# Optimization experiments

Hardware: AMD Instinct MI355X
Metric: run time of the kernel (lower is better)

Reference implementation:

```python
import jax, jax.numpy as jnp
import numpy as np

NUM_DOF = 7
NUM_STEPS = 100
T = 0.02
V_MAX, A_MAX, J_MAX, P_MAX = 1.0, 2.0, 5.0, 3.14
MAXITER = 20
RHO = 1.0
BATCH = 1024
HIDDEN = 1024
NVAR = NUM_DOF * NUM_STEPS            # 700
NUM_ACC = NUM_STEPS - 1
NUM_JERK = NUM_ACC - 1
NUM_POS = NUM_STEPS
NVC = 2 * NUM_STEPS * NUM_DOF         # vel constraints
NAC = 2 * NUM_ACC * NUM_DOF
NJC = 2 * NUM_JERK * NUM_DOF
NPC = 2 * NUM_POS * NUM_DOF
M_CON = NVC + NAC + NJC + NPC         # 5558 total constraints
OUT_DIM = 2 * NVAR + M_CON            # 6958 mlp output dim

def _build_mats():
    P_vel = np.eye(NUM_STEPS)
    P_acc = np.diff(P_vel, axis=0) / T
    P_jerk = np.diff(P_acc, axis=0) / T
    P_pos = np.cumsum(P_vel, axis=0) * T
    ud = lambda P: np.vstack((P, -P))
    I = np.eye(NUM_DOF)
    A_control = np.vstack([np.kron(I, ud(P)) for P in (P_vel, P_acc, P_jerk, P_pos)])
    bnd = np.zeros((1, NUM_STEPS)); bnd[0, 0] = 1.0
    A_eq = np.kron(I, bnd)
    cost = np.eye(NVAR) + RHO * (A_control.T @ A_control)  # A_projection = I
    Q = np.block([[cost, A_eq.T], [A_eq, np.zeros((NUM_DOF, NUM_DOF))]])
    Q_inv = np.linalg.inv(Q)
    return jnp.asarray(A_control, jnp.float32), jnp.asarray(Q_inv, jnp.float32)

A_CONTROL, Q_INV = _build_mats()


def setup_inputs() -> dict:
    key = jax.random.key(0)
    k1, k2, k3, k4, k5 = jax.random.split(key, 5)
    return {
        "input_nn": jax.random.normal(k1, (BATCH, NVAR), jnp.float32),
        "theta_init": jax.random.uniform(k2, (BATCH, 1), jnp.float32),
        "v_start": jax.random.normal(k3, (BATCH, NUM_DOF), jnp.float32),
        "W1": jax.random.normal(k4, (NVAR, HIDDEN), jnp.float32) / np.sqrt(NVAR).astype(np.float32),
        "b1": jnp.zeros((HIDDEN,), jnp.float32),
        "W2": jax.random.normal(k5, (HIDDEN, OUT_DIM), jnp.float32) / np.sqrt(HIDDEN).astype(np.float32),
        "b2": jnp.zeros((OUT_DIM,), jnp.float32),
    }


def reference(input_nn, theta_init, v_start, W1, b1, W2, b2):
    # robust normalization (torch.median on even batch = lower middle element)
    med = jnp.quantile(input_nn, 0.5, axis=0, method="lower")
    q1 = jnp.quantile(input_nn, 0.25, axis=0)
    q3 = jnp.quantile(input_nn, 0.75, axis=0)
    iqr = q3 - q1
    iqr = jnp.where(iqr == 0, jnp.asarray(1.0, iqr.dtype), iqr)
    inp_norm = (input_nn - med) / iqr

    # mlp decoder
    h = jax.nn.relu(inp_norm @ W1 + b1)
    out = h @ W2 + b2
    xi0 = out[:, :NVAR]
    lam0 = out[:, NVAR:2 * NVAR]
    s0 = jnp.maximum(0.0, out[:, 2 * NVAR:2 * NVAR + M_CON])

    xi_samples = input_nn[:, :NVAR]
    B = input_nn.shape[0]
    dt = input_nn.dtype
    b_control = jnp.concatenate([
        V_MAX * jnp.ones((B, NVC), dt),
        A_MAX * jnp.ones((B, NAC), dt),
        J_MAX * jnp.ones((B, NJC), dt),
        (-theta_init + P_MAX) * jnp.ones((B, NPC // 2), dt),
        (theta_init + P_MAX) * jnp.ones((B, NPC // 2), dt),
    ], axis=1)  # [B, M_CON]
    b_eq = v_start  # [B, num_dof]

    def step(carry, _):
        xi, lam, s = carry
        b_aug = b_control - s
        # lincost = -lamda - xi_samples - rho * A_control^T b_aug   (A_projection = I)
        lincost = -lam - xi_samples - RHO * (b_aug @ A_CONTROL)
        rhs = jnp.concatenate([-lincost, b_eq], axis=1)        # [B, nvar+dof]
        sol = rhs @ Q_INV.T
        xi_new = sol[:, :NVAR]
        Ax = xi_new @ A_CONTROL.T                              # [B, M_CON]
        s_new = jnp.maximum(0.0, b_control - Ax)
        res_vec = Ax - b_control + s_new
        res_norm = jnp.linalg.norm(res_vec, axis=1)
        lam_new = lam - RHO * (res_vec @ A_CONTROL)
        fp = jnp.linalg.norm(lam - lam_new, axis=1) + jnp.linalg.norm(s - s_new, axis=1)
        return (xi_new, lam_new, s_new), (res_norm, fp)

    (xi_f, _, _), (primal_res, fixed_res) = jax.lax.scan(step, (xi0, lam0, s0), None, length=MAXITER)
    avg_primal = jnp.sum(primal_res, axis=0) / MAXITER
    avg_fixed = jnp.sum(fixed_res, axis=0) / MAXITER
    return xi_f, avg_fixed, avg_primal, primal_res, fixed_res
```

## Files before the change

kernel.cpp:

```cpp
#include <hip/hip_runtime.h>

#define NVARS 700
#define MC    5558
#define MAXIT 20

typedef __attribute__((ext_vector_type(8))) short bf16x8;
typedef __attribute__((ext_vector_type(4))) float f32x4;

__device__ __forceinline__ ushort f2bf(float x) {
  unsigned u = __float_as_uint(x);
  return (ushort)((u + 0x7FFFu + ((u >> 16) & 1u)) >> 16);
}

__device__ __forceinline__ double Wfun(int a, int b) {
  if (a < 0 || a > 99 || b < 0 || b > 99) return 0.0;
  int d = a - b; if (d < 0) d = -d;
  int l = a < b ? a : b;
  const double iT2 = 2500.0;
  const double iT4 = 6250000.0;
  double w = 0.0;
  if (d == 0) {
    w = 3.0;
    w += 2.0 * iT2 * (double)((a <= 98 ? 1 : 0) + (a >= 1 ? 1 : 0));
    double dd = (double)(((a - 2) >= 0 && (a - 2) <= 97) ? 1 : 0)
              + 4.0 * (double)(((a - 1) >= 0 && (a - 1) <= 97) ? 1 : 0)
              + (double)((a <= 97) ? 1 : 0);
    w += 2.0 * iT4 * dd;
  } else if (d == 1) {
    w = -2.0 * iT2;
    double dd = -2.0 * (double)(((l - 1) >= 0 && (l - 1) <= 97) ? 1 : 0)
                - 2.0 * (double)((l <= 97) ? 1 : 0);
    w += 2.0 * iT4 * dd;
  } else if (d == 2) {
    w = 2.0 * iT4 * (double)((l <= 97) ? 1 : 0);
  }
  return w;
}

__global__ __launch_bounds__(128) void qinv_kernel(double* __restrict__ zbuf,
                                                   double* __restrict__ cid,
                                                   float* __restrict__ Qt)
{
  __shared__ double Bb[100][4];
  __shared__ double Gb[100][4];
  __shared__ double invd[100];
  int tid = threadIdx.x;
  for (int q = tid; q < 400; q += 128) {
    int i = q >> 2, k = q & 3;
    int j = i - k;
    double v = 0.0;
    if (j >= 0) {
      v = Wfun(i, j) - Wfun(i + 1, j) - Wfun(i, j + 1) + Wfun(i + 1, j + 1);
      if (k == 0) v += 2.0 * 0.02 * 0.02;
    }
    Bb[i][k] = v;
  }
  __syncthreads();
  if (tid == 0) {
    for (int i = 0; i < 100; ++i) {
      for (int k = 3; k >= 1; --k) {
        int j = i - k;
        if (j < 0) { Gb[i][k] = 0.0; continue; }
        double s = Bb[i][k];
        for (int m = k + 1; m <= 3; ++m)
          if (m <= i) s -= Gb[i][m] * Gb[j][m - k];
        Gb[i][k] = s * invd[j];
      }
      double s = Bb[i][0];
      for (int m = 1; m <= 3; ++m)
        if (m <= i) s -= Gb[i][m] * Gb[i][m];
      double g = sqrt(s);
      Gb[i][0] = g;
      invd[i] = 1.0 / g;
    }
  }
  __syncthreads();
  if (tid < 100) {
    int c = tid;
    double z0 = 0, z1 = 0, z2 = 0;
    for (int i = 0; i < 100; ++i) {
      double v = (i == c ? 1.0 : 0.0) - (i == (c - 1) ? 1.0 : 0.0);
      double s = v - Gb[i][1] * z0 - Gb[i][2] * z1 - Gb[i][3] * z2;
      double z = s * invd[i];
      zbuf[i * 128 + c] = z;
      z2 = z1; z1 = z0; z0 = z;
    }
    double y0 = 0, y1 = 0, y2 = 0;
    for (int i = 99; i >= 0; --i) {
      double s = zbuf[i * 128 + c];
      if (i + 1 <= 99) s -= Gb[i + 1][1] * y0;
      if (i + 2 <= 99) s -= Gb[i + 2][2] * y1;
      if (i + 3 <= 99) s -= Gb[i + 3][3] * y2;
      double y = s * invd[i];
      zbuf[i * 128 + c] = y;
      y2 = y1; y1 = y0; y0 = y;
    }
    double ym = 0.0;
    for (int i = 0; i < 100; ++i) {
      double y = zbuf[i * 128 + c];
      cid[i * 100 + c] = y - ym;
      ym = y;
    }
  }
  __syncthreads();
  double invs = 1.0 / cid[0];
  for (int q = tid; q < 101 * 100; q += 128) {
    int k = q / 100, i = q - (q / 100) * 100;
    double val;
    if (k < 100) val = cid[i * 100 + k] - cid[i * 100] * cid[k] * invs;
    else         val = cid[i * 100] * invs;
    Qt[k * 100 + i] = (float)val;
  }
}

__global__ __launch_bounds__(256) void quantile_kernel(const float* __restrict__ in,
                                                       float* __restrict__ med,
                                                       float* __restrict__ rinv)
{
  __shared__ float v[1024];
  int c = blockIdx.x, tid = threadIdx.x;
  for (int i = tid; i < 1024; i += 256) v[i] = in[i * NVARS + c];
  __syncthreads();
  for (int k = 2; k <= 1024; k <<= 1) {
    for (int j = k >> 1; j > 0; j >>= 1) {
      for (int i = tid; i < 1024; i += 256) {
        int ixj = i ^ j;
        if (ixj > i) {
          float a = v[i], b2 = v[ixj];
          bool up = ((i & k) == 0);
          if ((a > b2) == up) { v[i] = b2; v[ixj] = a; }
        }
      }
      __syncthreads();
    }
  }
  if (tid == 0) {
    float m  = v[511];
    float q1 = v[255] + 0.75f * (v[256] - v[255]);
    float q3 = v[767] + 0.25f * (v[768] - v[767]);
    float iq = q3 - q1;
    if (iq == 0.f) iq = 1.f;
    med[c] = m;
    rinv[c] = 1.f / iq;
  }
}

__global__ __launch_bounds__(256) void normalize_split(const float* __restrict__ in,
                                                       const float* __restrict__ med,
                                                       const float* __restrict__ rinv,
                                                       ushort* __restrict__ Ah,
                                                       ushort* __restrict__ Al)
{
  int idx = blockIdx.x * 256 + threadIdx.x;
  if (idx >= 1024 * 704) return;
  int r = idx / 704, c = idx - r * 704;
  float v = 0.f;
  if (c < 700) v = (in[r * NVARS + c] - med[c]) * rinv[c];
  ushort h = f2bf(v);
  float fh = __uint_as_float(((unsigned)h) << 16);
  Ah[idx] = h;
  Al[idx] = f2bf(v - fh);
}

__global__ __launch_bounds__(256) void tsplit(const float* __restrict__ src,
                                              int srows, int scols, int sld, int col0,
                                              ushort* __restrict__ dh,
                                              ushort* __restrict__ dl, int dld)
{
  __shared__ float tile[32][33];
  int k0 = blockIdx.x * 32, n0 = blockIdx.y * 32;
  int tx = threadIdx.x, ty = threadIdx.y;
  for (int i = ty; i < 32; i += 8) {
    int k = k0 + i, c = col0 + n0 + tx;
    tile[i][tx] = (k < srows && c < scols) ? src[(size_t)k * sld + c] : 0.f;
  }
  __syncthreads();
  for (int i = ty; i < 32; i += 8) {
    int n = n0 + i, k = k0 + tx;
    float v = tile[tx][i];
    ushort h = f2bf(v);
    float fh = __uint_as_float(((unsigned)h) << 16);
    dh[(size_t)n * dld + k] = h;
    dl[(size_t)n * dld + k] = f2bf(v - fh);
  }
}

template <int MODE>
__global__ __launch_bounds__(256) void gemm_mfma(
    const ushort* __restrict__ Agh, const ushort* __restrict__ Agl,
    const ushort* __restrict__ Bgh, const ushort* __restrict__ Bgl,
    const float* __restrict__ bias, int bias_n,
    float* __restrict__ Cf, ushort* __restrict__ Chi, ushort* __restrict__ Clo,
    int Kp, int ldc)
{
  __shared__ __align__(16) ushort Ash[128 * 40];
  __shared__ __align__(16) ushort Asl[128 * 40];
  __shared__ __align__(16) ushort Bsh[128 * 40];
  __shared__ __align__(16) ushort Bsl[128 * 40];

  const int t = threadIdx.x;
  const int srow = t >> 1;
  const int sc0 = (t & 1) * 2;
  const size_t bm = (size_t)blockIdx.y * 128;
  const size_t bn = (size_t)blockIdx.x * 128;

  const ushort* gAh = Agh + (bm + srow) * Kp + sc0 * 8;
  const ushort* gAl = Agl + (bm + srow) * Kp + sc0 * 8;
  const ushort* gBh = Bgh + (bn + srow) * Kp + sc0 * 8;
  const ushort* gBl = Bgl + (bn + srow) * Kp + sc0 * 8;

  const int w = t >> 6, lane = t & 63;
  const int wr = w >> 1, wc = w & 1;
  const int fr = lane & 15, fg = lane >> 4;

  f32x4 acc[4][4];
#pragma unroll
  for (int a = 0; a < 4; ++a)
#pragma unroll
    for (int b = 0; b < 4; ++b) acc[a][b] = (f32x4){0.f, 0.f, 0.f, 0.f};

  const int nk = Kp >> 5;
  uint4 rA0, rA1, rAl0, rAl1, rB0, rB1, rBl0, rBl1;
  {
    rA0  = *(const uint4*)(gAh);      rA1  = *(const uint4*)(gAh + 8);
    rAl0 = *(const uint4*)(gAl);      rAl1 = *(const uint4*)(gAl + 8);
    rB0  = *(const uint4*)(gBh);      rB1  = *(const uint4*)(gBh + 8);
    rBl0 = *(const uint4*)(gBl);      rBl1 = *(const uint4*)(gBl + 8);
  }
  const int woff = srow * 40 + sc0 * 8;

  for (int kt = 0;; ++kt) {
    __syncthreads();
    *(uint4*)&Ash[woff] = rA0;  *(uint4*)&Ash[woff + 8] = rA1;
    *(uint4*)&Asl[woff] = rAl0; *(uint4*)&Asl[woff + 8] = rAl1;
    *(uint4*)&Bsh[woff] = rB0;  *(uint4*)&Bsh[woff + 8] = rB1;
    *(uint4*)&Bsl[woff] = rBl0; *(uint4*)&Bsl[woff + 8] = rBl1;
    __syncthreads();
    if (kt + 1 < nk) {
      int ko = (kt + 1) * 32;
      rA0  = *(const uint4*)(gAh + ko);      rA1  = *(const uint4*)(gAh + ko + 8);
      rAl0 = *(const uint4*)(gAl + ko);      rAl1 = *(const uint4*)(gAl + ko + 8);
      rB0  = *(const uint4*)(gBh + ko);      rB1  = *(const uint4*)(gBh + ko + 8);
      rBl0 = *(const uint4*)(gBl + ko);      rBl1 = *(const uint4*)(gBl + ko + 8);
    }
    bf16x8 fah[4], fal[4], fbh[4], fbl[4];
#pragma unroll
    for (int mf = 0; mf < 4; ++mf) {
      int off = (wr * 64 + mf * 16 + fr) * 40 + fg * 8;
      fah[mf] = *(const bf16x8*)&Ash[off];
      fal[mf] = *(const bf16x8*)&Asl[off];
    }
#pragma unroll
    for (int nf = 0; nf < 4; ++nf) {
      int off = (wc * 64 + nf * 16 + fr) * 40 + fg * 8;
      fbh[nf] = *(const bf16x8*)&Bsh[off];
      fbl[nf] = *(const bf16x8*)&Bsl[off];
    }
#pragma unroll
    for (int mf = 0; mf < 4; ++mf)
#pragma unroll
      for (int nf = 0; nf < 4; ++nf) {
        acc[mf][nf] = __builtin_amdgcn_mfma_f32_16x16x32_bf16(fah[mf], fbh[nf], acc[mf][nf], 0, 0, 0);
        acc[mf][nf] = __builtin_amdgcn_mfma_f32_16x16x32_bf16(fah[mf], fbl[nf], acc[mf][nf], 0, 0, 0);
        acc[mf][nf] = __builtin_amdgcn_mfma_f32_16x16x32_bf16(fal[mf], fbh[nf], acc[mf][nf], 0, 0, 0);
      }
    if (kt + 1 >= nk) break;
  }

#pragma unroll
  for (int mf = 0; mf < 4; ++mf)
#pragma unroll
    for (int nf = 0; nf < 4; ++nf) {
      int col = (int)bn + wc * 64 + nf * 16 + fr;
      int rowb = (int)bm + wr * 64 + mf * 16 + fg * 4;
#pragma unroll
      for (int j = 0; j < 4; ++j) {
        int row = rowb + j;
        float v = acc[mf][nf][j];
        if (MODE == 0) {
          float bv = (col < bias_n) ? bias[col] : 0.f;
          Cf[(size_t)row * ldc + col] = v + bv;
        } else {
          float r = fmaxf(v + bias[col], 0.f);
          ushort h = f2bf(r);
          float fh = __uint_as_float(((unsigned)h) << 16);
          Chi[(size_t)row * ldc + col] = h;
          Clo[(size_t)row * ldc + col] = f2bf(r - fh);
        }
      }
    }
}

__global__ __launch_bounds__(256) void normalize_kernel(const float* __restrict__ in,
                                                        const float* __restrict__ med,
                                                        const float* __restrict__ rinv,
                                                        float* __restrict__ An)
{
  int idx = blockIdx.x * 256 + threadIdx.x;
  if (idx < 1024 * NVARS) {
    int c = idx % NVARS;
    An[idx] = (in[idx] - med[c]) * rinv[c];
  }
}

template <bool RELU>
__global__ __launch_bounds__(256) void gemm_kernel(const float* __restrict__ A, int lda,
                                                   const float* __restrict__ B, int ldb,
                                                   const float* __restrict__ bias,
                                                   float* __restrict__ C, int ldc,
                                                   int N, int K)
{
  __shared__ __align__(16) float As[16][68];
  __shared__ __align__(16) float Bs[16][64];
  int tid = threadIdx.x;
  int bm = blockIdx.y * 64, bn = blockIdx.x * 64;
  int tx = tid & 15, ty = tid >> 4;
  float acc[4][4] = {};
  for (int k0 = 0; k0 < K; k0 += 16) {
    {
      int q = tid * 4;
      int m = q >> 4, kk = q & 15;
      const float* ap = A + (size_t)(bm + m) * lda + k0;
#pragma unroll
      for (int s2 = 0; s2 < 4; ++s2) {
        int kc = kk + s2;
        As[kc][m] = (k0 + kc < K) ? ap[kc] : 0.f;
      }
    }
#pragma unroll
    for (int s2 = 0; s2 < 4; ++s2) {
      int q = tid + s2 * 256;
      int kk = q >> 6, n = q & 63;
      float val = 0.f;
      if (k0 + kk < K && bn + n < N) val = B[(size_t)(k0 + kk) * ldb + bn + n];
      Bs[kk][n] = val;
    }
    __syncthreads();
#pragma unroll
    for (int kk = 0; kk < 16; ++kk) {
      float4 av = *reinterpret_cast<const float4*>(&As[kk][ty * 4]);
      float4 bv = *reinterpret_cast<const float4*>(&Bs[kk][tx * 4]);
      acc[0][0] += av.x * bv.x; acc[0][1] += av.x * bv.y; acc[0][2] += av.x * bv.z; acc[0][3] += av.x * bv.w;
      acc[1][0] += av.y * bv.x; acc[1][1] += av.y * bv.y; acc[1][2] += av.y * bv.z; acc[1][3] += av.y * bv.w;
      acc[2][0] += av.z * bv.x; acc[2][1] += av.z * bv.y; acc[2][2] += av.z * bv.z; acc[2][3] += av.z * bv.w;
      acc[3][0] += av.w * bv.x; acc[3][1] += av.w * bv.y; acc[3][2] += av.w * bv.z; acc[3][3] += av.w * bv.w;
    }
    __syncthreads();
  }
#pragma unroll
  for (int i = 0; i < 4; ++i) {
    int m = bm + ty * 4 + i;
#pragma unroll
    for (int j = 0; j < 4; ++j) {
      int n = bn + tx * 4 + j;
      if (n < N) {
        float r = acc[i][j] + bias[n];
        if (RELU) r = fmaxf(r, 0.f);
        C[(size_t)m * ldc + n] = r;
      }
    }
  }
}

__device__ __forceinline__ float iscan(float v, int lane) {
#pragma unroll
  for (int off = 1; off < 64; off <<= 1) {
    float u = __shfl_up(v, off);
    v += (lane >= off) ? u : 0.f;
  }
  return v;
}

template <bool RES>
__device__ __forceinline__ float segw(const float* td, int pi, int mi) {
  if (!RES) return fmaxf(td[mi], 0.f) - fmaxf(td[pi], 0.f);
  else      return fmaxf(-td[pi], 0.f) - fmaxf(-td[mi], 0.f);
}

template <bool RES>
__device__ __forceinline__ float atop(const float* td, int i, float rc) {
  float u = segw<RES>(td, i, 100 + i);
  float ya = (i >= 1)  ? segw<RES>(td, 200 + i - 1, 299 + i - 1) : 0.f;
  float yb = (i <= 98) ? segw<RES>(td, 200 + i,     299 + i)     : 0.f;
  u += (ya - yb) * 50.f;
  float z2 = (i >= 2)             ? segw<RES>(td, 398 + i - 2, 496 + i - 2) : 0.f;
  float z1 = (i >= 1 && i <= 98)  ? segw<RES>(td, 398 + i - 1, 496 + i - 1) : 0.f;
  float z0 = (i <= 97)            ? segw<RES>(td, 398 + i,     496 + i)     : 0.f;
  u += (z2 - 2.f * z1 + z0) * 2500.f;
  u += 0.02f * rc;
  return u;
}

__global__ __launch_bounds__(448) void solver_kernel(const float* __restrict__ out2,
                                                     const float* __restrict__ input,
                                                     const float* __restrict__ theta,
                                                     const float* __restrict__ vstart,
                                                     const float* __restrict__ Qtg,
                                                     float* __restrict__ out, int ldo)
{
  __shared__ float t_l[7][794];
  __shared__ __align__(16) float ru_t[101][8];
  __shared__ float pm[4][700];
  __shared__ float part[7][20][3];
  __shared__ float prfp[40];

  const int b = blockIdx.x, tid = threadIdx.x;
  const int d = tid >> 6, l = tid & 63;
  const bool hi = (l < 36);
  const int i2 = 64 + l;
  float* td = &t_l[d][0];
  const float* orow = out2 + (size_t)b * ldo;
  const float* srow = orow + 700;
  const float th = theta[b];

  float lam0 = orow[d * 100 + l];
  float xs0  = input[(size_t)b * NVARS + d * 100 + l];
  float lam1 = 0.f, xs1 = 0.f;
  if (hi) {
    lam1 = orow[d * 100 + i2];
    xs1  = input[(size_t)b * NVARS + d * 100 + i2];
  }
  {
    int vb = d * 200, ab = 1400 + d * 198, jb = 2786 + d * 196, pb = 4158 + d * 200;
    td[l]       = fmaxf(srow[vb + l], 0.f);
    td[100 + l] = fmaxf(srow[vb + 100 + l], 0.f);
    if (l <= 98) { td[200 + l] = fmaxf(srow[ab + l], 0.f);      td[299 + l] = fmaxf(srow[ab + 99 + l], 0.f); }
    if (l <= 97) { td[398 + l] = fmaxf(srow[jb + l], 0.f);      td[496 + l] = fmaxf(srow[jb + 98 + l], 0.f); }
    td[594 + l] = fmaxf(srow[pb + l], 0.f);
    td[694 + l] = fmaxf(srow[pb + 100 + l], 0.f);
    if (hi) {
      td[i2]       = fmaxf(srow[vb + i2], 0.f);
      td[100 + i2] = fmaxf(srow[vb + 100 + i2], 0.f);
      if (l <= 34) { td[200 + i2] = fmaxf(srow[ab + i2], 0.f);  td[299 + i2] = fmaxf(srow[ab + 99 + i2], 0.f); }
      if (l <= 33) { td[398 + i2] = fmaxf(srow[jb + i2], 0.f);  td[496 + i2] = fmaxf(srow[jb + 98 + i2], 0.f); }
      td[594 + i2] = fmaxf(srow[pb + i2], 0.f);
      td[694 + i2] = fmaxf(srow[pb + 100 + i2], 0.f);
    }
  }
  if (l == 0) ru_t[100][d] = vstart[b * 7 + d];

  for (int it = 0; it < MAXIT; ++it) {
    {
      float pa0 = segw<false>(td, 594 + l, 694 + l);
      float pa1 = hi ? segw<false>(td, 594 + i2, 694 + i2) : 0.f;
      if (d == 3) { pa0 -= 2.f * th; if (hi) pa1 -= 2.f * th; }
      float s0i = iscan(pa0, l);
      float tot0 = __shfl(s0i, 63);
      float s1i = iscan(hi ? pa1 : 0.f, l) + tot0;
      float S = __shfl(s1i, 35);
      float rc0 = S - s0i + pa0;
      float ru0 = lam0 + xs0 + atop<false>(td, l, rc0);
      ru_t[l][d] = ru0;
      if (hi) {
        float rc1 = S - s1i + pa1;
        float ru1 = lam1 + xs1 + atop<false>(td, i2, rc1);
        ru_t[i2][d] = ru1;
      }
    }
    __syncthreads();

    {
      int kc = tid / 112, r = tid - kc * 112;
      if (r < 100) {
        float acc[7] = {0.f, 0.f, 0.f, 0.f, 0.f, 0.f, 0.f};
        int k0 = kc * 25, k1 = (kc == 3) ? 101 : k0 + 25;
        for (int k = k0; k < k1; ++k) {
          float qv = Qtg[k * 100 + r];
          float4 ra = *reinterpret_cast<const float4*>(&ru_t[k][0]);
          float4 rb = *reinterpret_cast<const float4*>(&ru_t[k][4]);
          acc[0] += qv * ra.x; acc[1] += qv * ra.y; acc[2] += qv * ra.z; acc[3] += qv * ra.w;
          acc[4] += qv * rb.x; acc[5] += qv * rb.y; acc[6] += qv * rb.z;
        }
#pragma unroll
        for (int dd = 0; dd < 7; ++dd) pm[kc][dd * 100 + r] = acc[dd];
      }
    }
    __syncthreads();
    {
      int p = tid;
      if (p < 700) { float v = pm[0][p] + pm[1][p] + pm[2][p] + pm[3][p]; pm[0][p] = v; }
      p = tid + 448;
      if (p < 700) { float v = pm[0][p] + pm[1][p] + pm[2][p] + pm[3][p]; pm[0][p] = v; }
    }
    __syncthreads();

    float r2 = 0.f, ds2 = 0.f, dl2 = 0.f;
    {
      const float* xid = &pm[0][d * 100];
      float x0 = xid[l], x1 = hi ? xid[i2] : 0.f;
      float c0i = iscan(x0, l);
      float tt0 = __shfl(c0i, 63);
      float c1i = iscan(hi ? x1 : 0.f, l) + tt0;
      float bp = (d <= 3) ? (3.14f - th) : (3.14f + th);
      float bm2 = (d < 3) ? (3.14f - th) : (3.14f + th);
#define UPD(idx, tnew) { int _ix = (idx); float _tn = (tnew); float _to = td[_ix]; \
      float _dd = fmaxf(_to, 0.f) - fmaxf(_tn, 0.f); ds2 += _dd * _dd; \
      float _rr = fmaxf(-_tn, 0.f); r2 += _rr * _rr; td[_ix] = _tn; }
      UPD(l, 1.f - x0) UPD(100 + l, 1.f + x0)
      if (hi) { UPD(i2, 1.f - x1) UPD(100 + i2, 1.f + x1) }
      if (l <= 98) { float a = (xid[l + 1] - x0) * 50.f; UPD(200 + l, 2.f - a) UPD(299 + l, 2.f + a) }
      if (hi && l <= 34) { float a = (xid[i2 + 1] - x1) * 50.f; UPD(200 + i2, 2.f - a) UPD(299 + i2, 2.f + a) }
      if (l <= 97) { float jr = (xid[l + 2] - 2.f * xid[l + 1] + x0) * 2500.f; UPD(398 + l, 5.f - jr) UPD(496 + l, 5.f + jr) }
      if (hi && l <= 33) { float jr = (xid[i2 + 2] - 2.f * xid[i2 + 1] + x1) * 2500.f; UPD(398 + i2, 5.f - jr) UPD(496 + i2, 5.f + jr) }
      UPD(594 + l, bp - 0.02f * c0i) UPD(694 + l, bm2 + 0.02f * c0i)
      if (hi) { UPD(594 + i2, bp - 0.02f * c1i) UPD(694 + i2, bm2 + 0.02f * c1i) }
#undef UPD
    }

    {
      float pa0 = segw<true>(td, 594 + l, 694 + l);
      float pa1 = hi ? segw<true>(td, 594 + i2, 694 + i2) : 0.f;
      float s0i = iscan(pa0, l);
      float tot0 = __shfl(s0i, 63);
      float s1i = iscan(hi ? pa1 : 0.f, l) + tot0;
      float S = __shfl(s1i, 35);
      float rc0 = S - s0i + pa0;
      float g0 = atop<true>(td, l, rc0);
      lam0 -= g0; dl2 += g0 * g0;
      if (hi) {
        float rc1 = S - s1i + pa1;
        float g1 = atop<true>(td, i2, rc1);
        lam1 -= g1; dl2 += g1 * g1;
      }
    }

#pragma unroll
    for (int o = 32; o > 0; o >>= 1) {
      r2  += __shfl_down(r2, o);
      ds2 += __shfl_down(ds2, o);
      dl2 += __shfl_down(dl2, o);
    }
    if (l == 0) { part[d][it][0] = r2; part[d][it][1] = ds2; part[d][it][2] = dl2; }
  }

  __syncthreads();
  {
    float* xout = out + (size_t)b * NVARS + d * 100;
    const float* xid = &pm[0][d * 100];
    xout[l] = xid[l];
    if (hi) xout[i2] = xid[i2];
  }
  if (tid < 20) {
    int it = tid;
    float R2 = 0.f, DS2 = 0.f, DL2 = 0.f;
    for (int dd = 0; dd < 7; ++dd) {
      R2 += part[dd][it][0]; DS2 += part[dd][it][1]; DL2 += part[dd][it][2];
    }
    float pr = sqrtf(R2), fp = sqrtf(DL2) + sqrtf(DS2);
    out[718848 + it * 1024 + b] = pr;
    out[739328 + it * 1024 + b] = fp;
    prfp[it] = pr; prfp[20 + it] = fp;
  }
  __syncthreads();
  if (tid == 0) {
    float ap = 0.f, af = 0.f;
    for (int it = 0; it < 20; ++it) { ap += prfp[it]; af += prfp[20 + it]; }
    out[716800 + b] = af / 20.f;
    out[717824 + b] = ap / 20.f;
  }
}

extern "C" void kernel_launch(void* const* d_in, const int* in_sizes, int n_in,
                              void* d_out, int out_size, void* d_ws, size_t ws_size,
                              hipStream_t stream) {
  (void)in_sizes; (void)n_in; (void)out_size;
  const float* input  = (const float*)d_in[0];
  const float* theta  = (const float*)d_in[1];
  const float* vstart = (const float*)d_in[2];
  const float* W1     = (const float*)d_in[3];
  const float* b1     = (const float*)d_in[4];
  const float* W2     = (const float*)d_in[5];
  const float* b2     = (const float*)d_in[6];
  float* out = (float*)d_out;

  double* wsd  = (double*)d_ws;
  double* zbuf = wsd;
  double* cid  = wsd + 12800;
  float* wsf  = (float*)d_ws;
  float* Qt   = wsf + 45600;
  float* med  = wsf + 55704;
  float* rinv = wsf + 56408;

  hipLaunchKernelGGL(qinv_kernel, dim3(1), dim3(128), 0, stream, zbuf, cid, Qt);
  hipLaunchKernelGGL(quantile_kernel, dim3(700), dim3(256), 0, stream, input, med, rinv);

  const size_t HHI = 57112, HLO = 581400, W2TH = 1105688, W2TL = 4316952,
               OUT2 = 7528216, NEED = 13950744;
  const size_t ANH = OUT2, ANL = OUT2 + 360448, W1TH = OUT2 + 720896, W1TL = OUT2 + 1081344;

  if (ws_size >= NEED * 4ull) {
    ushort* an_h  = (ushort*)(wsf + ANH);
    ushort* an_l  = (ushort*)(wsf + ANL);
    ushort* w1t_h = (ushort*)(wsf + W1TH);
    ushort* w1t_l = (ushort*)(wsf + W1TL);
    ushort* h_h   = (ushort*)(wsf + HHI);
    ushort* h_l   = (ushort*)(wsf + HLO);
    ushort* w2t_h = (ushort*)(wsf + W2TH);
    ushort* w2t_l = (ushort*)(wsf + W2TL);
    float*  out2  = wsf + OUT2;

    hipLaunchKernelGGL(normalize_split, dim3((1024 * 704 + 255) / 256), dim3(256), 0, stream,
                       input, med, rinv, an_h, an_l);
    hipLaunchKernelGGL(tsplit, dim3(22, 32), dim3(32, 8), 0, stream,
                       W1, 700, 1024, 1024, 0, w1t_h, w1t_l, 704);
    hipLaunchKernelGGL(tsplit, dim3(32, 196), dim3(32, 8), 0, stream,
                       W2, 1024, 6958, 6958, 700, w2t_h, w2t_l, 1024);
    hipLaunchKernelGGL((gemm_mfma<1>), dim3(8, 8), dim3(256), 0, stream,
                       an_h, an_l, w1t_h, w1t_l, b1, 1024,
                       (float*)nullptr, h_h, h_l, 704, 1024);
    hipLaunchKernelGGL((gemm_mfma<0>), dim3(49, 8), dim3(256), 0, stream,
                       h_h, h_l, w2t_h, w2t_l, b2 + 700, 6258,
                       out2, (ushort*)nullptr, (ushort*)nullptr, 1024, 6272);
    hipLaunchKernelGGL(solver_kernel, dim3(1024), dim3(448), 0, stream,
                       out2, input, theta, vstart, Qt, out, 6272);
  } else {
    float* An   = wsf + 57112;
    float* h    = wsf + 773912;
    float* out2 = wsf + 1822488;
    if (ws_size < (size_t)(1822488 + 6408192) * 4) return;
    hipLaunchKernelGGL(normalize_kernel, dim3(2800), dim3(256), 0, stream, input, med, rinv, An);
    hipLaunchKernelGGL((gemm_kernel<true>), dim3(16, 16), dim3(256), 0, stream,
                       An, NVARS, W1, 1024, b1, h, 1024, 1024, NVARS);
    hipLaunchKernelGGL((gemm_kernel<false>), dim3(98, 16), dim3(256), 0, stream,
                       h, 1024, W2 + 700, 6958, b2 + 700, out2, 6258, 6258, 1024);
    hipLaunchKernelGGL(solver_kernel, dim3(1024), dim3(448), 0, stream,
                       out2, input, theta, vstart, Qt, out, 6258);
  }
}
```

Before: 555.8 us.

## Keep solver slack state in registers and retile MFMA GEMMs for more blocks

The solver kernel no longer keeps its per-DOF slack arrays in shared memory. Each lane holds its constraint slacks in registers, neighbour values move through warp shuffles, and the A^T-apply phase computes both the s-weighted and residual-weighted terms in one fused pass, which also drops a redundant scan. Less shared memory plus __launch_bounds__(448,7) aims for higher occupancy. The MFMA GEMM is templated on tile size and launched with smaller tiles (64x64 and 128x64) to spread work over more blocks, at the cost of less data reuse per block.

New measurement: 776.7 us. 1.4x slower.

```diff
diff --git a/kernel.cpp b/kernel.cpp
--- a/kernel.cpp
+++ b/kernel.cpp
@@ -185,7 +185,7 @@
   }
 }
 
-template <int MODE>
+template <int BM, int BN, int MODE>
 __global__ __launch_bounds__(256) void gemm_mfma(
     const ushort* __restrict__ Agh, const ushort* __restrict__ Agl,
     const ushort* __restrict__ Bgh, const ushort* __restrict__ Bgl,
@@ -193,73 +193,82 @@
     float* __restrict__ Cf, ushort* __restrict__ Chi, ushort* __restrict__ Clo,
     int Kp, int ldc)
 {
-  __shared__ __align__(16) ushort Ash[128 * 40];
-  __shared__ __align__(16) ushort Asl[128 * 40];
-  __shared__ __align__(16) ushort Bsh[128 * 40];
-  __shared__ __align__(16) ushort Bsl[128 * 40];
+  constexpr int ACH = BM * 4 / 256;
+  constexpr int BCH = BN * 4 / 256;
+  constexpr int MF = BM / 32;
+  constexpr int NF = BN / 32;
+  __shared__ __align__(16) ushort Ash[BM * 40];
+  __shared__ __align__(16) ushort Asl[BM * 40];
+  __shared__ __align__(16) ushort Bsh[BN * 40];
+  __shared__ __align__(16) ushort Bsl[BN * 40];
 
   const int t = threadIdx.x;
-  const int srow = t >> 1;
-  const int sc0 = (t & 1) * 2;
-  const size_t bm = (size_t)blockIdx.y * 128;
-  const size_t bn = (size_t)blockIdx.x * 128;
-
-  const ushort* gAh = Agh + (bm + srow) * Kp + sc0 * 8;
-  const ushort* gAl = Agl + (bm + srow) * Kp + sc0 * 8;
-  const ushort* gBh = Bgh + (bn + srow) * Kp + sc0 * 8;
-  const ushort* gBl = Bgl + (bn + srow) * Kp + sc0 * 8;
+  const size_t bm = (size_t)blockIdx.y * BM;
+  const size_t bn = (size_t)blockIdx.x * BN;
+
+  size_t aoff[ACH]; int awo[ACH];
+#pragma unroll
+  for (int s = 0; s < ACH; ++s) {
+    int slot = t * ACH + s, row = slot >> 2, ch = slot & 3;
+    aoff[s] = (bm + row) * (size_t)Kp + ch * 8;
+    awo[s] = row * 40 + ch * 8;
+  }
+  size_t boff[BCH]; int bwo[BCH];
+#pragma unroll
+  for (int s = 0; s < BCH; ++s) {
+    int slot = t * BCH + s, row = slot >> 2, ch = slot & 3;
+    boff[s] = (bn + row) * (size_t)Kp + ch * 8;
+    bwo[s] = row * 40 + ch * 8;
+  }
 
   const int w = t >> 6, lane = t & 63;
   const int wr = w >> 1, wc = w & 1;
   const int fr = lane & 15, fg = lane >> 4;
 
-  f32x4 acc[4][4];
-#pragma unroll
-  for (int a = 0; a < 4; ++a)
-#pragma unroll
-    for (int b = 0; b < 4; ++b) acc[a][b] = (f32x4){0.f, 0.f, 0.f, 0.f};
+  f32x4 acc[MF][NF];
+#pragma unroll
+  for (int a = 0; a < MF; ++a)
+#pragma unroll
+    for (int b = 0; b < NF; ++b) acc[a][b] = (f32x4){0.f, 0.f, 0.f, 0.f};
 
   const int nk = Kp >> 5;
-  uint4 rA0, rA1, rAl0, rAl1, rB0, rB1, rBl0, rBl1;
-  {
-    rA0  = *(const uint4*)(gAh);      rA1  = *(const uint4*)(gAh + 8);
-    rAl0 = *(const uint4*)(gAl);      rAl1 = *(const uint4*)(gAl + 8);
-    rB0  = *(const uint4*)(gBh);      rB1  = *(const uint4*)(gBh + 8);
-    rBl0 = *(const uint4*)(gBl);      rBl1 = *(const uint4*)(gBl + 8);
-  }
-  const int woff = srow * 40 + sc0 * 8;
+  uint4 rAh[ACH], rAl[ACH], rBh[BCH], rBl[BCH];
+#pragma unroll
+  for (int s = 0; s < ACH; ++s) { rAh[s] = *(const uint4*)(Agh + aoff[s]); rAl[s] = *(const uint4*)(Agl + aoff[s]); }
+#pragma unroll
+  for (int s = 0; s < BCH; ++s) { rBh[s] = *(const uint4*)(Bgh + boff[s]); rBl[s] = *(const uint4*)(Bgl + boff[s]); }
 
   for (int kt = 0;; ++kt) {
     __syncthreads();
-    *(uint4*)&Ash[woff] = rA0;  *(uint4*)&Ash[woff + 8] = rA1;
-    *(uint4*)&Asl[woff] = rAl0; *(uint4*)&Asl[woff + 8] = rAl1;
-    *(uint4*)&Bsh[woff] = rB0;  *(uint4*)&Bsh[woff + 8] = rB1;
-    *(uint4*)&Bsl[woff] = rBl0; *(uint4*)&Bsl[woff + 8] = rBl1;
+#pragma unroll
+    for (int s = 0; s < ACH; ++s) { *(uint4*)&Ash[awo[s]] = rAh[s]; *(uint4*)&Asl[awo[s]] = rAl[s]; }
+#pragma unroll
+    for (int s = 0; s < BCH; ++s) { *(uint4*)&Bsh[bwo[s]] = rBh[s]; *(uint4*)&Bsl[bwo[s]] = rBl[s]; }
     __syncthreads();
     if (kt + 1 < nk) {
       int ko = (kt + 1) * 32;
-      rA0  = *(const uint4*)(gAh + ko);      rA1  = *(const uint4*)(gAh + ko + 8);
-      rAl0 = *(const uint4*)(gAl + ko);      rAl1 = *(const uint4*)(gAl + ko + 8);
-      rB0  = *(const uint4*)(gBh + ko);      rB1  = *(const uint4*)(gBh + ko + 8);
-      rBl0 = *(const uint4*)(gBl + ko);      rBl1 = *(const uint4*)(gBl + ko + 8);
-    }
-    bf16x8 fah[4], fal[4], fbh[4], fbl[4];
-#pragma unroll
-    for (int mf = 0; mf < 4; ++mf) {
-      int off = (wr * 64 + mf * 16 + fr) * 40 + fg * 8;
+#pragma unroll
+      for (int s = 0; s < ACH; ++s) { rAh[s] = *(const uint4*)(Agh + aoff[s] + ko); rAl[s] = *(const uint4*)(Agl + aoff[s] + ko); }
+#pragma unroll
+      for (int s = 0; s < BCH; ++s) { rBh[s] = *(const uint4*)(Bgh + boff[s] + ko); rBl[s] = *(const uint4*)(Bgl + boff[s] + ko); }
+    }
+    bf16x8 fah[MF], fal[MF], fbh[NF], fbl[NF];
+#pragma unroll
+    for (int mf = 0; mf < MF; ++mf) {
+      int off = (wr * (BM / 2) + mf * 16 + fr) * 40 + fg * 8;
       fah[mf] = *(const bf16x8*)&Ash[off];
       fal[mf] = *(const bf16x8*)&Asl[off];
     }
 #pragma unroll
-    for (int nf = 0; nf < 4; ++nf) {
-      int off = (wc * 64 + nf * 16 + fr) * 40 + fg * 8;
+    for (int nf = 0; nf < NF; ++nf) {
+      int off = (wc * (BN / 2) + nf * 16 + fr) * 40 + fg * 8;
       fbh[nf] = *(const bf16x8*)&Bsh[off];
       fbl[nf] = *(const bf16x8*)&Bsl[off];
     }
 #pragma unroll
-    for (int mf = 0; mf < 4; ++mf)
-#pragma unroll
-      for (int nf = 0; nf < 4; ++nf) {
+    for (int mf = 0; mf < MF; ++mf)
+#pragma unroll
+      for (int nf = 0; nf < NF; ++nf) {
         acc[mf][nf] = __builtin_amdgcn_mfma_f32_16x16x32_bf16(fah[mf], fbh[nf], acc[mf][nf], 0, 0, 0);
         acc[mf][nf] = __builtin_amdgcn_mfma_f32_16x16x32_bf16(fah[mf], fbl[nf], acc[mf][nf], 0, 0, 0);
         acc[mf][nf] = __builtin_amdgcn_mfma_f32_16x16x32_bf16(fal[mf], fbh[nf], acc[mf][nf], 0, 0, 0);
@@ -268,11 +277,11 @@
   }
 
 #pragma unroll
-  for (int mf = 0; mf < 4; ++mf)
-#pragma unroll
-    for (int nf = 0; nf < 4; ++nf) {
-      int col = (int)bn + wc * 64 + nf * 16 + fr;
-      int rowb = (int)bm + wr * 64 + mf * 16 + fg * 4;
+  for (int mf = 0; mf < MF; ++mf)
+#pragma unroll
+    for (int nf = 0; nf < NF; ++nf) {
+      int col = (int)bn + wc * (BN / 2) + nf * 16 + fr;
+      int rowb = (int)bm + wr * (BM / 2) + mf * 16 + fg * 4;
 #pragma unroll
       for (int j = 0; j < 4; ++j) {
         int row = rowb + j;
@@ -371,35 +380,72 @@
   return v;
 }
 
-template <bool RES>
-__device__ __forceinline__ float segw(const float* td, int pi, int mi) {
-  if (!RES) return fmaxf(td[mi], 0.f) - fmaxf(td[pi], 0.f);
-  else      return fmaxf(-td[pi], 0.f) - fmaxf(-td[mi], 0.f);
-}
-
-template <bool RES>
-__device__ __forceinline__ float atop(const float* td, int i, float rc) {
-  float u = segw<RES>(td, i, 100 + i);
-  float ya = (i >= 1)  ? segw<RES>(td, 200 + i - 1, 299 + i - 1) : 0.f;
-  float yb = (i <= 98) ? segw<RES>(td, 200 + i,     299 + i)     : 0.f;
-  u += (ya - yb) * 50.f;
-  float z2 = (i >= 2)             ? segw<RES>(td, 398 + i - 2, 496 + i - 2) : 0.f;
-  float z1 = (i >= 1 && i <= 98)  ? segw<RES>(td, 398 + i - 1, 496 + i - 1) : 0.f;
-  float z0 = (i <= 97)            ? segw<RES>(td, 398 + i,     496 + i)     : 0.f;
-  u += (z2 - 2.f * z1 + z0) * 2500.f;
-  u += 0.02f * rc;
-  return u;
-}
-
-__global__ __launch_bounds__(448) void solver_kernel(const float* __restrict__ out2,
-                                                     const float* __restrict__ input,
-                                                     const float* __restrict__ theta,
-                                                     const float* __restrict__ vstart,
-                                                     const float* __restrict__ Qtg,
-                                                     float* __restrict__ out, int ldo)
-{
-  __shared__ float t_l[7][794];
-  __shared__ __align__(16) float ru_t[101][8];
+struct TR {
+  float vp0, vm0, vp1, vm1;
+  float ap0, am0, ap1, am1;
+  float jp0, jm0, jp1, jm1;
+  float pp0, pm0, pp1, pm1;
+};
+
+__device__ __forceinline__ void wpair(float tp, float tm, float& ws, float& wr) {
+  float a = fmaxf(tp, 0.f), b = fmaxf(tm, 0.f);
+  ws = b - a;
+  wr = (tm - tp) - ws;
+}
+
+__device__ __forceinline__ void w_phase(const TR& t, int l, bool hi, float dth,
+                                        float& os0, float& os1, float& or0, float& or1)
+{
+  float vs0, vr0, vs1, vr1, ys0, yr0, ys1, yr1;
+  float zs0, zr0, zs1, zr1, ps0, pr0, ps1, pr1;
+  wpair(t.vp0, t.vm0, vs0, vr0);
+  wpair(t.ap0, t.am0, ys0, yr0);
+  wpair(t.jp0, t.jm0, zs0, zr0);
+  wpair(t.pp0, t.pm0, ps0, pr0);
+  if (hi) { wpair(t.vp1, t.vm1, vs1, vr1); wpair(t.pp1, t.pm1, ps1, pr1); }
+  else    { vs1 = vr1 = ps1 = pr1 = 0.f; }
+  if (hi && l <= 34) { wpair(t.ap1, t.am1, ys1, yr1); } else { ys1 = yr1 = 0.f; }
+  if (hi && l <= 33) { wpair(t.jp1, t.jm1, zs1, zr1); } else { zs1 = zr1 = 0.f; }
+
+  const int lm1 = (l + 63) & 63, lm2 = (l + 62) & 63;
+  float u1ys0 = __shfl(ys0, lm1), u1ys1 = __shfl(ys1, lm1);
+  float u1zs0 = __shfl(zs0, lm1), u1zs1 = __shfl(zs1, lm1);
+  float u2zs0 = __shfl(zs0, lm2), u2zs1 = __shfl(zs1, lm2);
+  float u1yr0 = __shfl(yr0, lm1), u1yr1 = __shfl(yr1, lm1);
+  float u1zr0 = __shfl(zr0, lm1), u1zr1 = __shfl(zr1, lm1);
+  float u2zr0 = __shfl(zr0, lm2), u2zr1 = __shfl(zr1, lm2);
+
+  float pa0s = ps0 + dth;
+  float pa1s = hi ? ps1 + dth : 0.f;
+  float pa0r = pr0;
+  float pa1r = hi ? pr1 : 0.f;
+  float s0s = iscan(pa0s, l);
+  float s0r = iscan(pa0r, l);
+  float tots = __shfl(s0s, 63), totr = __shfl(s0r, 63);
+  float s1s = iscan(pa1s, l) + tots;
+  float s1r = iscan(pa1r, l) + totr;
+  float Ss = __shfl(s1s, 35), Sr = __shfl(s1r, 35);
+  float rc0s = Ss - s0s + pa0s, rc1s = Ss - s1s + pa1s;
+  float rc0r = Sr - s0r + pa0r, rc1r = Sr - s1r + pa1r;
+
+  float ym1s0 = l ? u1ys0 : 0.f, zm1s0 = l ? u1zs0 : 0.f, zm2s0 = (l >= 2) ? u2zs0 : 0.f;
+  float ym1r0 = l ? u1yr0 : 0.f, zm1r0 = l ? u1zr0 : 0.f, zm2r0 = (l >= 2) ? u2zr0 : 0.f;
+  os0 = vs0 + 50.f * (ym1s0 - ys0) + 2500.f * (zm2s0 - 2.f * zm1s0 + zs0) + 0.02f * rc0s;
+  or0 = vr0 + 50.f * (ym1r0 - yr0) + 2500.f * (zm2r0 - 2.f * zm1r0 + zr0) + 0.02f * rc0r;
+  float ym1s1 = l ? u1ys1 : u1ys0, zm1s1 = l ? u1zs1 : u1zs0, zm2s1 = (l >= 2) ? u2zs1 : u2zs0;
+  float ym1r1 = l ? u1yr1 : u1yr0, zm1r1 = l ? u1zr1 : u1zr0, zm2r1 = (l >= 2) ? u2zr1 : u2zr0;
+  os1 = vs1 + 50.f * (ym1s1 - ys1) + 2500.f * (zm2s1 - 2.f * zm1s1 + zs1) + 0.02f * rc1s;
+  or1 = vr1 + 50.f * (ym1r1 - yr1) + 2500.f * (zm2r1 - 2.f * zm1r1 + zr1) + 0.02f * rc1r;
+}
+
+__global__ __launch_bounds__(448, 7) void solver_kernel(const float* __restrict__ out2,
+                                                        const float* __restrict__ input,
+                                                        const float* __restrict__ theta,
+                                                        const float* __restrict__ vstart,
+                                                        const float* __restrict__ Qtg,
+                                                        float* __restrict__ out, int ldo)
+{
+  __shared__ __align__(16) float ru_t[101][12];
   __shared__ float pm[4][700];
   __shared__ float part[7][20][3];
   __shared__ float prfp[40];
@@ -408,57 +454,45 @@
   const int d = tid >> 6, l = tid & 63;
   const bool hi = (l < 36);
   const int i2 = 64 + l;
-  float* td = &t_l[d][0];
+  const float th = theta[b];
+  const float dth = (d == 3) ? -2.f * th : 0.f;
+  const float bp  = (d <= 3) ? (3.14f - th) : (3.14f + th);
+  const float bm2 = (d <  3) ? (3.14f - th) : (3.14f + th);
   const float* orow = out2 + (size_t)b * ldo;
   const float* srow = orow + 700;
-  const float th = theta[b];
 
   float lam0 = orow[d * 100 + l];
   float xs0  = input[(size_t)b * NVARS + d * 100 + l];
-  float lam1 = 0.f, xs1 = 0.f;
-  if (hi) {
-    lam1 = orow[d * 100 + i2];
-    xs1  = input[(size_t)b * NVARS + d * 100 + i2];
-  }
+  float lam1 = hi ? orow[d * 100 + i2] : 0.f;
+  float xs1  = hi ? input[(size_t)b * NVARS + d * 100 + i2] : 0.f;
+
+  TR t;
   {
-    int vb = d * 200, ab = 1400 + d * 198, jb = 2786 + d * 196, pb = 4158 + d * 200;
-    td[l]       = fmaxf(srow[vb + l], 0.f);
-    td[100 + l] = fmaxf(srow[vb + 100 + l], 0.f);
-    if (l <= 98) { td[200 + l] = fmaxf(srow[ab + l], 0.f);      td[299 + l] = fmaxf(srow[ab + 99 + l], 0.f); }
-    if (l <= 97) { td[398 + l] = fmaxf(srow[jb + l], 0.f);      td[496 + l] = fmaxf(srow[jb + 98 + l], 0.f); }
-    td[594 + l] = fmaxf(srow[pb + l], 0.f);
-    td[694 + l] = fmaxf(srow[pb + 100 + l], 0.f);
-    if (hi) {
-      td[i2]       = fmaxf(srow[vb + i2], 0.f);
-      td[100 + i2] = fmaxf(srow[vb + 100 + i2], 0.f);
-      if (l <= 34) { td[200 + i2] = fmaxf(srow[ab + i2], 0.f);  td[299 + i2] = fmaxf(srow[ab + 99 + i2], 0.f); }
-      if (l <= 33) { td[398 + i2] = fmaxf(srow[jb + i2], 0.f);  td[496 + i2] = fmaxf(srow[jb + 98 + i2], 0.f); }
-      td[594 + i2] = fmaxf(srow[pb + i2], 0.f);
-      td[694 + i2] = fmaxf(srow[pb + 100 + i2], 0.f);
-    }
+    const int vb = d * 200, ab = 1400 + d * 198, jb = 2786 + d * 196, pb = 4158 + d * 200;
+    t.vp0 = fmaxf(srow[vb + l], 0.f);        t.vm0 = fmaxf(srow[vb + 100 + l], 0.f);
+    t.ap0 = fmaxf(srow[ab + l], 0.f);        t.am0 = fmaxf(srow[ab + 99 + l], 0.f);
+    t.jp0 = fmaxf(srow[jb + l], 0.f);        t.jm0 = fmaxf(srow[jb + 98 + l], 0.f);
+    t.pp0 = fmaxf(srow[pb + l], 0.f);        t.pm0 = fmaxf(srow[pb + 100 + l], 0.f);
+    t.vp1 = hi        ? fmaxf(srow[vb + i2], 0.f)      : 0.f;
+    t.vm1 = hi        ? fmaxf(srow[vb + 100 + i2], 0.f) : 0.f;
+    t.ap1 = (l <= 34) ? fmaxf(srow[ab + i2], 0.f)      : 0.f;
+    t.am1 = (l <= 34) ? fmaxf(srow[ab + 99 + i2], 0.f) : 0.f;
+    t.jp1 = (l <= 33) ? fmaxf(srow[jb + i2], 0.f)      : 0.f;
+    t.jm1 = (l <= 33) ? fmaxf(srow[jb + 98 + i2], 0.f) : 0.f;
+    t.pp1 = hi        ? fmaxf(srow[pb + i2], 0.f)      : 0.f;
+    t.pm1 = hi        ? fmaxf(srow[pb + 100 + i2], 0.f) : 0.f;
   }
   if (l == 0) ru_t[100][d] = vstart[b * 7 + d];
 
+  {
+    float os0, os1, or0, or1;
+    w_phase(t, l, hi, dth, os0, os1, or0, or1);
+    ru_t[l][d] = lam0 + xs0 + os0;
+    if (hi) ru_t[i2][d] = lam1 + xs1 + os1;
+  }
+
   for (int it = 0; it < MAXIT; ++it) {
-    {
-      float pa0 = segw<false>(td, 594 + l, 694 + l);
-      float pa1 = hi ? segw<false>(td, 594 + i2, 694 + i2) : 0.f;
-      if (d == 3) { pa0 -= 2.f * th; if (hi) pa1 -= 2.f * th; }
-      float s0i = iscan(pa0, l);
-      float tot0 = __shfl(s0i, 63);
-      float s1i = iscan(hi ? pa1 : 0.f, l) + tot0;
-      float S = __shfl(s1i, 35);
-      float rc0 = S - s0i + pa0;
-      float ru0 = lam0 + xs0 + atop<false>(td, l, rc0);
-      ru_t[l][d] = ru0;
-      if (hi) {
-        float rc1 = S - s1i + pa1;
-        float ru1 = lam1 + xs1 + atop<false>(td, i2, rc1);
-        ru_t[i2][d] = ru1;
-      }
-    }
     __syncthreads();
-
     {
       int kc = tid / 112, r = tid - kc * 112;
       if (r < 100) {
@@ -487,40 +521,44 @@
     float r2 = 0.f, ds2 = 0.f, dl2 = 0.f;
     {
       const float* xid = &pm[0][d * 100];
-      float x0 = xid[l], x1 = hi ? xid[i2] : 0.f;
-      float c0i = iscan(x0, l);
-      float tt0 = __shfl(c0i, 63);
-      float c1i = iscan(hi ? x1 : 0.f, l) + tt0;
-      float bp = (d <= 3) ? (3.14f - th) : (3.14f + th);
-      float bm2 = (d < 3) ? (3.14f - th) : (3.14f + th);
-#define UPD(idx, tnew) { int _ix = (idx); float _tn = (tnew); float _to = td[_ix]; \
-      float _dd = fmaxf(_to, 0.f) - fmaxf(_tn, 0.f); ds2 += _dd * _dd; \
-      float _rr = fmaxf(-_tn, 0.f); r2 += _rr * _rr; td[_ix] = _tn; }
-      UPD(l, 1.f - x0) UPD(100 + l, 1.f + x0)
-      if (hi) { UPD(i2, 1.f - x1) UPD(100 + i2, 1.f + x1) }
-      if (l <= 98) { float a = (xid[l + 1] - x0) * 50.f; UPD(200 + l, 2.f - a) UPD(299 + l, 2.f + a) }
-      if (hi && l <= 34) { float a = (xid[i2 + 1] - x1) * 50.f; UPD(200 + i2, 2.f - a) UPD(299 + i2, 2.f + a) }
-      if (l <= 97) { float jr = (xid[l + 2] - 2.f * xid[l + 1] + x0) * 2500.f; UPD(398 + l, 5.f - jr) UPD(496 + l, 5.f + jr) }
-      if (hi && l <= 33) { float jr = (xid[i2 + 2] - 2.f * xid[i2 + 1] + x1) * 2500.f; UPD(398 + i2, 5.f - jr) UPD(496 + i2, 5.f + jr) }
-      UPD(594 + l, bp - 0.02f * c0i) UPD(694 + l, bm2 + 0.02f * c0i)
-      if (hi) { UPD(594 + i2, bp - 0.02f * c1i) UPD(694 + i2, bm2 + 0.02f * c1i) }
-#undef UPD
+      float x0 = xid[l];
+      float x1 = hi ? xid[i2] : 0.f;
+      const int lp1 = (l + 1) & 63, lp2 = (l + 2) & 63;
+      float d1x0 = __shfl(x0, lp1), d1x1 = __shfl(x1, lp1);
+      float d2x0 = __shfl(x0, lp2), d2x1 = __shfl(x1, lp2);
+      float xp1_0 = (l == 63) ? d1x1 : d1x0;
+      float xp2_0 = (l >= 62) ? d2x1 : d2x0;
+      float xp1_1 = d1x1, xp2_1 = d2x1;
+      float c0 = iscan(x0, l);
+      float tt = __shfl(c0, 63);
+      float c1 = iscan(hi ? x1 : 0.f, l) + tt;
+#define NU(tp_, tm_, np_, nm_) { \
+      float sop = fmaxf(tp_, 0.f), som = fmaxf(tm_, 0.f); \
+      float snp = fmaxf(np_, 0.f), snm = fmaxf(nm_, 0.f); \
+      float e1 = sop - snp, e2 = som - snm; ds2 += e1 * e1 + e2 * e2; \
+      float q1 = snp - (np_), q2 = snm - (nm_); r2 += q1 * q1 + q2 * q2; \
+      tp_ = np_; tm_ = nm_; }
+      { float np = 1.f - x0, nm = 1.f + x0; NU(t.vp0, t.vm0, np, nm) }
+      { float a = 50.f * (xp1_0 - x0); float np = 2.f - a, nm = 2.f + a; NU(t.ap0, t.am0, np, nm) }
+      { float j = 2500.f * (xp2_0 - 2.f * xp1_0 + x0); float np = 5.f - j, nm = 5.f + j; NU(t.jp0, t.jm0, np, nm) }
+      { float np = bp - 0.02f * c0, nm = bm2 + 0.02f * c0; NU(t.pp0, t.pm0, np, nm) }
+      if (hi) {
+        { float np = 1.f - x1, nm = 1.f + x1; NU(t.vp1, t.vm1, np, nm) }
+        { float np = bp - 0.02f * c1, nm = bm2 + 0.02f * c1; NU(t.pp1, t.pm1, np, nm) }
+      }
+      if (l <= 34) { float a = 50.f * (xp1_1 - x1); float np = 2.f - a, nm = 2.f + a; NU(t.ap1, t.am1, np, nm) }
+      if (l <= 33) { float j = 2500.f * (xp2_1 - 2.f * xp1_1 + x1); float np = 5.f - j, nm = 5.f + j; NU(t.jp1, t.jm1, np, nm) }
+#undef NU
     }
 
     {
-      float pa0 = segw<true>(td, 594 + l, 694 + l);
-      float pa1 = hi ? segw<true>(td, 594 + i2, 694 + i2) : 0.f;
-      float s0i = iscan(pa0, l);
-      float tot0 = __shfl(s0i, 63);
-      float s1i = iscan(hi ? pa1 : 0.f, l) + tot0;
-      float S = __shfl(s1i, 35);
-      float rc0 = S - s0i + pa0;
-      float g0 = atop<true>(td, l, rc0);
-      lam0 -= g0; dl2 += g0 * g0;
+      float os0, os1, or0, or1;
+      w_phase(t, l, hi, dth, os0, os1, or0, or1);
+      lam0 -= or0; dl2 += or0 * or0;
+      ru_t[l][d] = lam0 + xs0 + os0;
       if (hi) {
-        float rc1 = S - s1i + pa1;
-        float g1 = atop<true>(td, i2, rc1);
-        lam1 -= g1; dl2 += g1 * g1;
+        lam1 -= or1; dl2 += or1 * or1;
+        ru_t[i2][d] = lam1 + xs1 + os1;
       }
     }
 
@@ -605,10 +643,10 @@
                        W1, 700, 1024, 1024, 0, w1t_h, w1t_l, 704);
     hipLaunchKernelGGL(tsplit, dim3(32, 196), dim3(32, 8), 0, stream,
                        W2, 1024, 6958, 6958, 700, w2t_h, w2t_l, 1024);
-    hipLaunchKernelGGL((gemm_mfma<1>), dim3(8, 8), dim3(256), 0, stream,
+    hipLaunchKernelGGL((gemm_mfma<64, 64, 1>), dim3(16, 16), dim3(256), 0, stream,
                        an_h, an_l, w1t_h, w1t_l, b1, 1024,
                        (float*)nullptr, h_h, h_l, 704, 1024);
-    hipLaunchKernelGGL((gemm_mfma<0>), dim3(49, 8), dim3(256), 0, stream,
+    hipLaunchKernelGGL((gemm_mfma<128, 64, 0>), dim3(98, 8), dim3(256), 0, stream,
                        h_h, h_l, w2t_h, w2t_l, b2 + 700, 6258,
                        out2, (ushort*)nullptr, (ushort*)nullptr, 1024, 6272);
     hipLaunchKernelGGL(solver_kernel, dim3(1024), dim3(448), 0, stream,
```
